# Kernel optimization log

Measured on AMD Instinct MI355X. Metric: run time of the kernel, lower is better.

The kernel has to match this reference:

```python
import jax, jax.numpy as jnp
import numpy as np

EPS = 1e-6  # torch GaussianNLLLoss default eps


def _linear_params(key, in_size, out_size):
    # torch nn.Linear default init: U(-1/sqrt(in), 1/sqrt(in)) for W and b
    kw, kb = jax.random.split(key)
    bound = 1.0 / np.sqrt(in_size)
    W = jax.random.uniform(kw, (out_size, in_size), minval=-bound, maxval=bound, dtype=jnp.float32)
    b = jax.random.uniform(kb, (out_size,), minval=-bound, maxval=bound, dtype=jnp.float32)
    return W, b


def setup_inputs() -> dict:
    key = jax.random.key(0)
    B, IN, H = 32768, 512, 512
    ks = jax.random.split(key, 6)
    x = jax.random.normal(ks[0], (B, IN), dtype=jnp.float32)
    y = jax.random.normal(ks[1], (B, IN), dtype=jnp.float32)
    W_mu_x, b_mu_x = _linear_params(ks[2], IN, H)
    W_sg_x, b_sg_x = _linear_params(ks[3], IN, H)
    W_mu_y, b_mu_y = _linear_params(ks[4], IN, H)
    W_sg_y, b_sg_y = _linear_params(ks[5], IN, H)
    return {"x": x, "y": y,
            "W_mu_x": W_mu_x, "b_mu_x": b_mu_x,
            "W_sg_x": W_sg_x, "b_sg_x": b_sg_x,
            "W_mu_y": W_mu_y, "b_mu_y": b_mu_y,
            "W_sg_y": W_sg_y, "b_sg_y": b_sg_y}


def _gaussian_nll(xi, mean, var):
    # torch GaussianNLLLoss (full=False, reduction='mean'):
    # mean over features of 0.5*(log(max(var,eps)) + (xi-mean)^2/max(var,eps))
    v = jnp.maximum(var, EPS)
    return 0.5 * jnp.mean(jnp.log(v) + (xi - mean) ** 2 / v)


def _sample_row(key, mx, my, vx, vy):
    # rejection sampling: draw u~U(0,1), xi~U(-1,1); accept when u >= q(xi)
    def cond(c):
        return jnp.logical_not(c[2])

    def body(c):
        k = c[0]
        k, k1, k2 = jax.random.split(k, 3)
        u = jax.random.uniform(k1, dtype=jnp.float32)
        xi = 2.0 * jax.random.uniform(k2, dtype=jnp.float32) - 1.0
        q = _gaussian_nll(xi, mx, vx) * _gaussian_nll(xi, my, vy)
        return (k, xi, u >= q)

    _, xi, _ = jax.lax.while_loop(cond, body, (key, jnp.float32(0.0), jnp.bool_(False)))
    return xi


def reference(x, y, W_mu_x, b_mu_x, W_sg_x, b_sg_x, W_mu_y, b_mu_y, W_sg_y, b_sg_y):
    mean_x = x @ W_mu_x.T + b_mu_x          # [B, H]
    mean_y = y @ W_mu_y.T + b_mu_y          # [B, H]
    std_x = jnp.exp(x @ W_sg_x.T + b_sg_x)  # [B, H] (used as 'var' in GaussianNLLLoss)
    std_y = jnp.exp(y @ W_sg_y.T + b_sg_y)  # [B, H]
    B = x.shape[0]
    keys = jax.random.split(jax.random.key(42), B)
    X = jax.vmap(_sample_row)(keys, mean_x, mean_y, std_x, std_y)  # [B]
    return jnp.clip(X, 1e-5, 10.0)
```

## Files before the change

kernel.cpp:

```cpp
#include <hip/hip_runtime.h>
#include <stdint.h>
#include <math.h>


typedef _Float16 f16;
typedef __attribute__((ext_vector_type(8))) _Float16 f16x8;
typedef __attribute__((ext_vector_type(4))) float f32x4;

#define SX 16.0f
#define SW 1024.0f
#define INV_S (1.0f / 16384.0f)
#define LOG_EPS (-13.815510557964274f)
#define PLANE 262144
#define WS_NEED (4u * 2u * PLANE * 2u)

#define KC_S   512
#define CJ_S   8192
#define WV_S   16384
#define CG_S   65536
#define HILO_S 262144
#define MAT_S  524288

struct U2 { uint32_t a, b; };

__device__ __forceinline__ uint32_t rotl(uint32_t v, int d) {
  return (v << d) | (v >> (32 - d));
}

__device__ __forceinline__ U2 tf2x32(uint32_t k0, uint32_t k1, uint32_t x0, uint32_t x1) {
  const uint32_t k2 = k0 ^ k1 ^ 0x1BD11BDAu;
  x0 += k0; x1 += k1;
#define TFR(r) { x0 += x1; x1 = rotl(x1, r); x1 ^= x0; }
  TFR(13) TFR(15) TFR(26) TFR(6)
  x0 += k1; x1 += k2 + 1u;
  TFR(17) TFR(29) TFR(16) TFR(24)
  x0 += k2; x1 += k0 + 2u;
  TFR(13) TFR(15) TFR(26) TFR(6)
  x0 += k0; x1 += k1 + 3u;
  TFR(17) TFR(29) TFR(16) TFR(24)
  x0 += k1; x1 += k2 + 4u;
  TFR(13) TFR(15) TFR(26) TFR(6)
  x0 += k2; x1 += k0 + 5u;
#undef TFR
  U2 r; r.a = x0; r.b = x1; return r;
}

__device__ __forceinline__ float bits_to_u01(uint32_t b) {
  return __uint_as_float((b >> 9) | 0x3f800000u) - 1.0f;
}

__global__ __launch_bounds__(256) void convert_w_kernel(
    const float* __restrict__ w0, const float* __restrict__ w1,
    const float* __restrict__ w2, const float* __restrict__ w3,
    f16* __restrict__ ws)
{
  const int t = blockIdx.x * 256 + threadIdx.x;
  const int mat = t >> 15;
  const int r = t & 32767;
  const int lane = r & 63;
  const int kc = (r >> 6) & 15;
  const int cj = (r >> 10) & 1;
  const int wv = (r >> 11) & 3;
  const int cg = (r >> 13) & 3;
  const int ln = lane & 15, quad = lane >> 4;
  const int row = cg * 128 + wv * 32 + cj * 16 + ln;
  const int k0 = kc * 32 + quad * 8;
  const float* W = (mat == 0) ? w0 : (mat == 1) ? w1 : (mat == 2) ? w2 : w3;
  const float* p = W + (size_t)row * 512 + k0;
  const float4 va = *(const float4*)p;
  const float4 vb = *(const float4*)(p + 4);
  const float a[8] = {va.x, va.y, va.z, va.w, vb.x, vb.y, vb.z, vb.w};
  f16x8 h, l;
#pragma unroll
  for (int i = 0; i < 8; ++i) {
    const float ai = a[i] * SW;
    const f16 hi = (f16)ai;
    h[i] = hi;
    l[i] = (f16)(ai - (float)hi);
  }
  f16* dst = ws + (size_t)mat * MAT_S + (size_t)cg * CG_S + (size_t)wv * WV_S
                + (size_t)cj * CJ_S + (size_t)kc * KC_S + (size_t)lane * 8;
  *(f16x8*)dst = h;
  *(f16x8*)(dst + HILO_S) = l;
}

__device__ __forceinline__ int swz_off(int row, int quad) {
  return row * 32 + ((quad ^ ((row >> 1) & 3)) << 3);
}

__global__ __launch_bounds__(256, 2)
void mfma_proposal_kernel(const float* __restrict__ gx, const float* __restrict__ gy,
                          const float* __restrict__ bmux, const float* __restrict__ bsgx,
                          const float* __restrict__ bmuy, const float* __restrict__ bsgy,
                          const f16* __restrict__ ws, float* __restrict__ out)
{
  __shared__ f16 Xh[64 * 32], Xl[64 * 32];
  __shared__ double red[4][64][8];

  const int tid = threadIdx.x;
  const int lane = tid & 63;
  const int w = tid >> 6;
  const int ln = lane & 15;
  const int quad = lane >> 4;
  const int r0 = blockIdx.x * 64;

  const int xrow = tid >> 2;
  const int xs4 = tid & 3;
  const int xslot = (xs4 ^ ((xrow >> 1) & 3)) << 3;

  for (int i = tid; i < 4 * 64 * 8; i += 256) (&red[0][0][0])[i] = 0.0;

  const f16* wbase = ws + (size_t)w * WV_S + (size_t)lane * 8;

  float4 xr0, xr1;
  auto load_xr = [&](int n) {
    const float* Xg = (n >> 6) ? gy : gx;
    const float* xp = Xg + (size_t)(r0 + xrow) * 512 + (n & 15) * 32 + xs4 * 8;
    xr0 = *(const float4*)(xp);
    xr1 = *(const float4*)(xp + 4);
  };

  auto write_x = [&]() {
    float a0 = xr0.x * SX, a1 = xr0.y * SX, a2 = xr0.z * SX, a3 = xr0.w * SX;
    float a4 = xr1.x * SX, a5 = xr1.y * SX, a6 = xr1.z * SX, a7 = xr1.w * SX;
    f16 h0 = (f16)a0, h1 = (f16)a1, h2 = (f16)a2, h3 = (f16)a3;
    f16 h4 = (f16)a4, h5 = (f16)a5, h6 = (f16)a6, h7 = (f16)a7;
    *(f16x8*)&Xh[xrow * 32 + xslot] = (f16x8){h0, h1, h2, h3, h4, h5, h6, h7};
    *(f16x8*)&Xl[xrow * 32 + xslot] =
        (f16x8){(f16)(a0 - (float)h0), (f16)(a1 - (float)h1),
                (f16)(a2 - (float)h2), (f16)(a3 - (float)h3),
                (f16)(a4 - (float)h4), (f16)(a5 - (float)h5),
                (f16)(a6 - (float)h6), (f16)(a7 - (float)h7)};
  };

  auto load_W = [&](int n, f16x8 (&B)[4][2]) {
    const int kc = n & 15, cg = (n >> 4) & 3, d = n >> 6;
    const f16* base = wbase + (size_t)(d * 2) * MAT_S + (size_t)cg * CG_S
                            + (size_t)kc * KC_S;
#pragma unroll
    for (int p = 0; p < 4; ++p)
#pragma unroll
      for (int cj = 0; cj < 2; ++cj)
        B[p][cj] = *(const f16x8*)(base + (size_t)(p >> 1) * MAT_S
                                        + (size_t)(p & 1) * HILO_S
                                        + (size_t)cj * CJ_S);
  };

  f16x8 Ba[4][2], Bb[4][2];
  f32x4 accm[4][2], accv[4][2];

  load_xr(0);
  load_W(0, Ba);

  auto round_fn = [&](int rid, f16x8 (&Bc)[4][2], f16x8 (&Bn)[4][2]) {
    const int kc = rid & 15;
    const int cg = (rid >> 4) & 3;
    const int dist = rid >> 6;

    if (kc == 0) {
#pragma unroll
      for (int ri = 0; ri < 4; ++ri)
#pragma unroll
        for (int cj = 0; cj < 2; ++cj) {
          accm[ri][cj] = (f32x4)0.0f;
          accv[ri][cj] = (f32x4)0.0f;
        }
    }

    __syncthreads();
    write_x();
    __syncthreads();

    if (rid + 1 < 128) {
      load_xr(rid + 1);
      load_W(rid + 1, Bn);
    }

    f16x8 ah[4], al[4];
#pragma unroll
    for (int ri = 0; ri < 4; ++ri) {
      const int off = swz_off(ri * 16 + ln, quad);
      ah[ri] = *(const f16x8*)&Xh[off];
      al[ri] = *(const f16x8*)&Xl[off];
    }
#pragma unroll
    for (int cj = 0; cj < 2; ++cj) {
      const f16x8 bhm = Bc[0][cj];
      const f16x8 blm = Bc[1][cj];
      const f16x8 bhv = Bc[2][cj];
      const f16x8 blv = Bc[3][cj];
#pragma unroll
      for (int ri = 0; ri < 4; ++ri) {
        accm[ri][cj] = __builtin_amdgcn_mfma_f32_16x16x32_f16(al[ri], bhm, accm[ri][cj], 0, 0, 0);
        accm[ri][cj] = __builtin_amdgcn_mfma_f32_16x16x32_f16(ah[ri], blm, accm[ri][cj], 0, 0, 0);
        accm[ri][cj] = __builtin_amdgcn_mfma_f32_16x16x32_f16(ah[ri], bhm, accm[ri][cj], 0, 0, 0);
        accv[ri][cj] = __builtin_amdgcn_mfma_f32_16x16x32_f16(al[ri], bhv, accv[ri][cj], 0, 0, 0);
        accv[ri][cj] = __builtin_amdgcn_mfma_f32_16x16x32_f16(ah[ri], blv, accv[ri][cj], 0, 0, 0);
        accv[ri][cj] = __builtin_amdgcn_mfma_f32_16x16x32_f16(ah[ri], bhv, accv[ri][cj], 0, 0, 0);
      }
    }

    if (kc == 15) {
      const float* bmu = dist ? bmuy : bmux;
      const float* bsg = dist ? bsgy : bsgx;
      float bm0 = bmu[cg * 128 + w * 32 + ln];
      float bm1 = bmu[cg * 128 + w * 32 + 16 + ln];
      float bv0 = bsg[cg * 128 + w * 32 + ln];
      float bv1 = bsg[cg * 128 + w * 32 + 16 + ln];
#pragma unroll
      for (int ri = 0; ri < 4; ++ri) {
#pragma unroll
        for (int g = 0; g < 4; ++g) {
          float pA = 0.f, pI = 0.f, pM = 0.f, pQ = 0.f;
#pragma unroll
          for (int cj = 0; cj < 2; ++cj) {
            const float m = accm[ri][cj][g] * INV_S + (cj ? bm1 : bm0);
            const float s = accv[ri][cj][g] * INV_S + (cj ? bv1 : bv0);
            const float vv = fmaxf(expf(s), 1e-6f);
            const float lg = fmaxf(s, LOG_EPS);
            const float iv = __builtin_amdgcn_rcpf(vv);
            pA += lg;
            pI += iv;
            pM += m * iv;
            pQ += m * m * iv;
          }
#pragma unroll
          for (int msk = 1; msk < 16; msk <<= 1) {
            pA += __shfl_xor(pA, msk);
            pI += __shfl_xor(pI, msk);
            pM += __shfl_xor(pM, msk);
            pQ += __shfl_xor(pQ, msk);
          }
          if (ln == 0) {
            double* rr = &red[w][ri * 16 + quad * 4 + g][dist * 4];
            rr[0] += (double)pA; rr[1] += (double)pI;
            rr[2] += (double)pM; rr[3] += (double)pQ;
          }
        }
      }
    }
  };

  for (int rr = 0; rr < 64; ++rr) {
    round_fn(rr * 2,     Ba, Bb);
    round_fn(rr * 2 + 1, Bb, Ba);
  }

  __syncthreads();

  if (tid < 64) {
    const int grow = r0 + tid;
    double Ax = 0, Ix = 0, Mx = 0, Qx = 0, Ay = 0, Iy = 0, My = 0, Qy = 0;
#pragma unroll
    for (int s = 0; s < 4; ++s) {
      Ax += red[s][tid][0]; Ix += red[s][tid][1];
      Mx += red[s][tid][2]; Qx += red[s][tid][3];
      Ay += red[s][tid][4]; Iy += red[s][tid][5];
      My += red[s][tid][6]; Qy += red[s][tid][7];
    }

    U2 key = tf2x32(0u, 42u, 0u, (uint32_t)grow);

    float xi = 0.0f;
    bool done = false;
    for (int it = 0; it < 100000 && !done; ++it) {
      const U2 kn = tf2x32(key.a, key.b, 0u, 0u);
      const U2 k1 = tf2x32(key.a, key.b, 0u, 1u);
      const U2 k2 = tf2x32(key.a, key.b, 0u, 2u);
      const U2 ru = tf2x32(k1.a, k1.b, 0u, 0u);
      const U2 rx = tf2x32(k2.a, k2.b, 0u, 0u);
      const float u  = bits_to_u01(ru.a ^ ru.b);
      const float u2 = bits_to_u01(rx.a ^ rx.b);
      xi = 2.0f * u2 - 1.0f;
      const double dxi = (double)xi;
      const double nx = (0.5 / 512.0) * (Ax + Qx + dxi * (dxi * Ix - 2.0 * Mx));
      const double ny = (0.5 / 512.0) * (Ay + Qy + dxi * (dxi * Iy - 2.0 * My));
      done = ((double)u >= nx * ny);
      key = kn;
    }
    out[grow] = fminf(fmaxf(xi, 1e-5f), 10.0f);
  }
}

__global__ __launch_bounds__(256, 1)
void fused_proposal_vec(const float* __restrict__ gx, const float* __restrict__ gy,
                        const float* __restrict__ Wmux, const float* __restrict__ bmux,
                        const float* __restrict__ Wsgx, const float* __restrict__ bsgx,
                        const float* __restrict__ Wmuy, const float* __restrict__ bmuy,
                        const float* __restrict__ Wsgy, const float* __restrict__ bsgy,
                        float* __restrict__ out)
{
  __shared__ float Xs[16][68];
  __shared__ float Wms[16][132];
  __shared__ float Wss[16][132];
  __shared__ double red[64][8];

  const int tid = threadIdx.x;
  const int tx = tid & 15;
  const int ty = tid >> 4;
  const int r0 = blockIdx.x * 64;
  const int lr = tid >> 2;
  const int q4 = (tid & 3) << 2;

  for (int i = tid; i < 64 * 8; i += 256) ((double*)red)[i] = 0.0;

  for (int ph = 0; ph < 8; ++ph) {
    const int dist = ph >> 2;
    const int c0 = (ph & 3) * 128;
    const float* __restrict__ Xg = dist ? gy : gx;
    const float* __restrict__ Wm = dist ? Wmuy : Wmux;
    const float* __restrict__ Wv = dist ? Wsgy : Wsgx;
    const float* __restrict__ bm = dist ? bmuy : bmux;
    const float* __restrict__ bv = dist ? bsgy : bsgx;

    float am[4][8], av[4][8];
#pragma unroll
    for (int r = 0; r < 4; ++r)
#pragma unroll
      for (int c = 0; c < 8; ++c) { am[r][c] = 0.0f; av[r][c] = 0.0f; }

    const float* xp  = Xg + (size_t)(r0 + lr) * 512 + q4;
    const float* mp0 = Wm + (size_t)(c0 + lr) * 512 + q4;
    const float* mp1 = Wm + (size_t)(c0 + lr + 64) * 512 + q4;
    const float* vp0 = Wv + (size_t)(c0 + lr) * 512 + q4;
    const float* vp1 = Wv + (size_t)(c0 + lr + 64) * 512 + q4;

    float4 xa = *(const float4*)(xp);
    float4 ma = *(const float4*)(mp0);
    float4 mb = *(const float4*)(mp1);
    float4 va = *(const float4*)(vp0);
    float4 vb = *(const float4*)(vp1);

    for (int t = 0; t < 32; ++t) {
      __syncthreads();
#define ST4(arr, col, v) { arr[q4+0][col]=v.x; arr[q4+1][col]=v.y; arr[q4+2][col]=v.z; arr[q4+3][col]=v.w; }
      ST4(Xs,  lr, xa)
      ST4(Wms, lr, ma)  ST4(Wms, lr + 64, mb)
      ST4(Wss, lr, va)  ST4(Wss, lr + 64, vb)
#undef ST4
      __syncthreads();
      if (t + 1 < 32) {
        const int ko = (t + 1) * 16;
        xa = *(const float4*)(xp + ko);
        ma = *(const float4*)(mp0 + ko);
        mb = *(const float4*)(mp1 + ko);
        va = *(const float4*)(vp0 + ko);
        vb = *(const float4*)(vp1 + ko);
      }
#pragma unroll
      for (int kk = 0; kk < 16; ++kk) {
        const float4 x0 = *(const float4*)&Xs[kk][ty * 4];
        const float4 m0 = *(const float4*)&Wms[kk][tx * 4];
        const float4 m1 = *(const float4*)&Wms[kk][tx * 4 + 64];
        const float4 v0 = *(const float4*)&Wss[kk][tx * 4];
        const float4 v1 = *(const float4*)&Wss[kk][tx * 4 + 64];
        const float xr[4] = {x0.x, x0.y, x0.z, x0.w};
        const float wm[8] = {m0.x, m0.y, m0.z, m0.w, m1.x, m1.y, m1.z, m1.w};
        const float wv[8] = {v0.x, v0.y, v0.z, v0.w, v1.x, v1.y, v1.z, v1.w};
#pragma unroll
        for (int r = 0; r < 4; ++r)
#pragma unroll
          for (int c = 0; c < 8; ++c) {
            am[r][c] = fmaf(xr[r], wm[c], am[r][c]);
            av[r][c] = fmaf(xr[r], wv[c], av[r][c]);
          }
      }
    }

    float bmr[8], bvr[8];
#pragma unroll
    for (int c = 0; c < 4; ++c) {
      bmr[c]     = bm[c0 + tx * 4 + c];
      bmr[4 + c] = bm[c0 + 64 + tx * 4 + c];
      bvr[c]     = bv[c0 + tx * 4 + c];
      bvr[4 + c] = bv[c0 + 64 + tx * 4 + c];
    }
#pragma unroll
    for (int r = 0; r < 4; ++r) {
      float pA = 0.f, pI = 0.f, pM = 0.f, pQ = 0.f;
#pragma unroll
      for (int c = 0; c < 8; ++c) {
        const float m = am[r][c] + bmr[c];
        const float s = av[r][c] + bvr[c];
        const float v = fmaxf(expf(s), 1e-6f);
        const float lg = fmaxf(s, LOG_EPS);
        const float inv = __builtin_amdgcn_rcpf(v);
        pA += lg; pI += inv; pM += m * inv; pQ += m * m * inv;
      }
#pragma unroll
      for (int msk = 1; msk < 16; msk <<= 1) {
        pA += __shfl_xor(pA, msk);
        pI += __shfl_xor(pI, msk);
        pM += __shfl_xor(pM, msk);
        pQ += __shfl_xor(pQ, msk);
      }
      if (tx == 0) {
        double* rr = &red[ty * 4 + r][dist * 4];
        rr[0] += (double)pA; rr[1] += (double)pI;
        rr[2] += (double)pM; rr[3] += (double)pQ;
      }
    }
  }

  __syncthreads();

  if (tid < 64) {
    const int grow = r0 + tid;
    const double Ax = red[tid][0], Ix = red[tid][1], Mx = red[tid][2], Qx = red[tid][3];
    const double Ay = red[tid][4], Iy = red[tid][5], My = red[tid][6], Qy = red[tid][7];
    U2 key = tf2x32(0u, 42u, 0u, (uint32_t)grow);
    float xi = 0.0f;
    bool done = false;
    for (int it = 0; it < 100000 && !done; ++it) {
      const U2 kn = tf2x32(key.a, key.b, 0u, 0u);
      const U2 k1 = tf2x32(key.a, key.b, 0u, 1u);
      const U2 k2 = tf2x32(key.a, key.b, 0u, 2u);
      const U2 ru = tf2x32(k1.a, k1.b, 0u, 0u);
      const U2 rx = tf2x32(k2.a, k2.b, 0u, 0u);
      const float u  = bits_to_u01(ru.a ^ ru.b);
      const float u2 = bits_to_u01(rx.a ^ rx.b);
      xi = 2.0f * u2 - 1.0f;
      const double dxi = (double)xi;
      const double nx = (0.5 / 512.0) * (Ax + Qx + dxi * (dxi * Ix - 2.0 * Mx));
      const double ny = (0.5 / 512.0) * (Ay + Qy + dxi * (dxi * Iy - 2.0 * My));
      done = ((double)u >= nx * ny);
      key = kn;
    }
    out[grow] = fminf(fmaxf(xi, 1e-5f), 10.0f);
  }
}

extern "C" void kernel_launch(void* const* d_in, const int* in_sizes, int n_in,
                              void* d_out, int out_size, void* d_ws, size_t ws_size,
                              hipStream_t stream) {
  const float* x    = (const float*)d_in[0];
  const float* y    = (const float*)d_in[1];
  const float* Wmux = (const float*)d_in[2];
  const float* bmux = (const float*)d_in[3];
  const float* Wsgx = (const float*)d_in[4];
  const float* bsgx = (const float*)d_in[5];
  const float* Wmuy = (const float*)d_in[6];
  const float* bmuy = (const float*)d_in[7];
  const float* Wsgy = (const float*)d_in[8];
  const float* bsgy = (const float*)d_in[9];
  (void)in_sizes; (void)n_in; (void)out_size;

  if (ws_size >= (size_t)WS_NEED) {
    convert_w_kernel<<<512, 256, 0, stream>>>(Wmux, Wsgx, Wmuy, Wsgy, (f16*)d_ws);
    mfma_proposal_kernel<<<512, 256, 0, stream>>>(
        x, y, bmux, bsgx, bmuy, bsgy, (const f16*)d_ws, (float*)d_out);
  } else {
    fused_proposal_vec<<<512, 256, 0, stream>>>(
        x, y, Wmux, bmux, Wsgx, bsgx, Wmuy, bmuy, Wsgy, bsgy, (float*)d_out);
  }
}
```

Baseline: 367.8 us.

## Halve rows per block, double-buffer X tile, raise occupancy to four blocks

Each block now handles 32 rows instead of 64, with twice as many blocks and launch bounds raised to four blocks per CU. The X tile in LDS is double-buffered so only one barrier is needed per round, and register double-buffering of W fragments is replaced by per-round loads. The intent is more waves to hide latency and fewer barriers, at the cost of halved W reuse per block and therefore more L2/global weight traffic.

```diff
diff --git a/kernel.cpp b/kernel.cpp
--- a/kernel.cpp
+++ b/kernel.cpp
@@ -88,78 +88,70 @@
   return row * 32 + ((quad ^ ((row >> 1) & 3)) << 3);
 }
 
-__global__ __launch_bounds__(256, 2)
+__global__ __launch_bounds__(256, 4)
 void mfma_proposal_kernel(const float* __restrict__ gx, const float* __restrict__ gy,
                           const float* __restrict__ bmux, const float* __restrict__ bsgx,
                           const float* __restrict__ bmuy, const float* __restrict__ bsgy,
                           const f16* __restrict__ ws, float* __restrict__ out)
 {
-  __shared__ f16 Xh[64 * 32], Xl[64 * 32];
-  __shared__ double red[4][64][8];
+  __shared__ f16 Xh[2][32 * 32], Xl[2][32 * 32];
+  __shared__ double red[4][32][8];
 
   const int tid = threadIdx.x;
   const int lane = tid & 63;
   const int w = tid >> 6;
   const int ln = lane & 15;
   const int quad = lane >> 4;
-  const int r0 = blockIdx.x * 64;
-
-  const int xrow = tid >> 2;
+  const int r0 = blockIdx.x * 32;
+
+  const int xrow = (tid & 127) >> 2;
   const int xs4 = tid & 3;
   const int xslot = (xs4 ^ ((xrow >> 1) & 3)) << 3;
 
-  for (int i = tid; i < 4 * 64 * 8; i += 256) (&red[0][0][0])[i] = 0.0;
+  for (int i = tid; i < 4 * 32 * 8; i += 256) (&red[0][0][0])[i] = 0.0;
 
   const f16* wbase = ws + (size_t)w * WV_S + (size_t)lane * 8;
 
   float4 xr0, xr1;
   auto load_xr = [&](int n) {
-    const float* Xg = (n >> 6) ? gy : gx;
-    const float* xp = Xg + (size_t)(r0 + xrow) * 512 + (n & 15) * 32 + xs4 * 8;
-    xr0 = *(const float4*)(xp);
-    xr1 = *(const float4*)(xp + 4);
+    if (w < 2) {
+      const float* Xg = (n >> 6) ? gy : gx;
+      const float* xp = Xg + (size_t)(r0 + xrow) * 512 + (n & 15) * 32 + xs4 * 8;
+      xr0 = *(const float4*)(xp);
+      xr1 = *(const float4*)(xp + 4);
+    }
   };
 
-  auto write_x = [&]() {
-    float a0 = xr0.x * SX, a1 = xr0.y * SX, a2 = xr0.z * SX, a3 = xr0.w * SX;
-    float a4 = xr1.x * SX, a5 = xr1.y * SX, a6 = xr1.z * SX, a7 = xr1.w * SX;
-    f16 h0 = (f16)a0, h1 = (f16)a1, h2 = (f16)a2, h3 = (f16)a3;
-    f16 h4 = (f16)a4, h5 = (f16)a5, h6 = (f16)a6, h7 = (f16)a7;
-    *(f16x8*)&Xh[xrow * 32 + xslot] = (f16x8){h0, h1, h2, h3, h4, h5, h6, h7};
-    *(f16x8*)&Xl[xrow * 32 + xslot] =
-        (f16x8){(f16)(a0 - (float)h0), (f16)(a1 - (float)h1),
-                (f16)(a2 - (float)h2), (f16)(a3 - (float)h3),
-                (f16)(a4 - (float)h4), (f16)(a5 - (float)h5),
-                (f16)(a6 - (float)h6), (f16)(a7 - (float)h7)};
+  auto write_x = [&](int buf) {
+    if (w < 2) {
+      float a0 = xr0.x * SX, a1 = xr0.y * SX, a2 = xr0.z * SX, a3 = xr0.w * SX;
+      float a4 = xr1.x * SX, a5 = xr1.y * SX, a6 = xr1.z * SX, a7 = xr1.w * SX;
+      f16 h0 = (f16)a0, h1 = (f16)a1, h2 = (f16)a2, h3 = (f16)a3;
+      f16 h4 = (f16)a4, h5 = (f16)a5, h6 = (f16)a6, h7 = (f16)a7;
+      *(f16x8*)&Xh[buf][xrow * 32 + xslot] = (f16x8){h0, h1, h2, h3, h4, h5, h6, h7};
+      *(f16x8*)&Xl[buf][xrow * 32 + xslot] =
+          (f16x8){(f16)(a0 - (float)h0), (f16)(a1 - (float)h1),
+                  (f16)(a2 - (float)h2), (f16)(a3 - (float)h3),
+                  (f16)(a4 - (float)h4), (f16)(a5 - (float)h5),
+                  (f16)(a6 - (float)h6), (f16)(a7 - (float)h7)};
+    }
   };
 
-  auto load_W = [&](int n, f16x8 (&B)[4][2]) {
-    const int kc = n & 15, cg = (n >> 4) & 3, d = n >> 6;
-    const f16* base = wbase + (size_t)(d * 2) * MAT_S + (size_t)cg * CG_S
-                            + (size_t)kc * KC_S;
-#pragma unroll
-    for (int p = 0; p < 4; ++p)
-#pragma unroll
-      for (int cj = 0; cj < 2; ++cj)
-        B[p][cj] = *(const f16x8*)(base + (size_t)(p >> 1) * MAT_S
-                                        + (size_t)(p & 1) * HILO_S
-                                        + (size_t)cj * CJ_S);
-  };
-
-  f16x8 Ba[4][2], Bb[4][2];
-  f32x4 accm[4][2], accv[4][2];
+  f32x4 accm[2][2], accv[2][2];
 
   load_xr(0);
-  load_W(0, Ba);
-
-  auto round_fn = [&](int rid, f16x8 (&Bc)[4][2], f16x8 (&Bn)[4][2]) {
+  write_x(0);
+  load_xr(1);
+
+  for (int rid = 0; rid < 128; ++rid) {
+    const int cb = rid & 1;
     const int kc = rid & 15;
     const int cg = (rid >> 4) & 3;
     const int dist = rid >> 6;
 
     if (kc == 0) {
 #pragma unroll
-      for (int ri = 0; ri < 4; ++ri)
+      for (int ri = 0; ri < 2; ++ri)
 #pragma unroll
         for (int cj = 0; cj < 2; ++cj) {
           accm[ri][cj] = (f32x4)0.0f;
@@ -168,29 +160,38 @@
     }
 
     __syncthreads();
-    write_x();
-    __syncthreads();
-
-    if (rid + 1 < 128) {
-      load_xr(rid + 1);
-      load_W(rid + 1, Bn);
-    }
-
-    f16x8 ah[4], al[4];
-#pragma unroll
-    for (int ri = 0; ri < 4; ++ri) {
+
+    if (rid + 1 < 128) write_x(cb ^ 1);
+    if (rid + 2 < 128) load_xr(rid + 2);
+
+    f16x8 B[4][2];
+    {
+      const f16* base = wbase + (size_t)(dist * 2) * MAT_S + (size_t)cg * CG_S
+                              + (size_t)kc * KC_S;
+#pragma unroll
+      for (int p = 0; p < 4; ++p)
+#pragma unroll
+        for (int cj = 0; cj < 2; ++cj)
+          B[p][cj] = *(const f16x8*)(base + (size_t)(p >> 1) * MAT_S
+                                          + (size_t)(p & 1) * HILO_S
+                                          + (size_t)cj * CJ_S);
+    }
+
+    f16x8 ah[2], al[2];
+#pragma unroll
+    for (int ri = 0; ri < 2; ++ri) {
       const int off = swz_off(ri * 16 + ln, quad);
-      ah[ri] = *(const f16x8*)&Xh[off];
-      al[ri] = *(const f16x8*)&Xl[off];
+      ah[ri] = *(const f16x8*)&Xh[cb][off];
+      al[ri] = *(const f16x8*)&Xl[cb][off];
     }
 #pragma unroll
     for (int cj = 0; cj < 2; ++cj) {
-      const f16x8 bhm = Bc[0][cj];
-      const f16x8 blm = Bc[1][cj];
-      const f16x8 bhv = Bc[2][cj];
-      const f16x8 blv = Bc[3][cj];
-#pragma unroll
-      for (int ri = 0; ri < 4; ++ri) {
+      const f16x8 bhm = B[0][cj];
+      const f16x8 blm = B[1][cj];
+      const f16x8 bhv = B[2][cj];
+      const f16x8 blv = B[3][cj];
+#pragma unroll
+      for (int ri = 0; ri < 2; ++ri) {
         accm[ri][cj] = __builtin_amdgcn_mfma_f32_16x16x32_f16(al[ri], bhm, accm[ri][cj], 0, 0, 0);
         accm[ri][cj] = __builtin_amdgcn_mfma_f32_16x16x32_f16(ah[ri], blm, accm[ri][cj], 0, 0, 0);
         accm[ri][cj] = __builtin_amdgcn_mfma_f32_16x16x32_f16(ah[ri], bhm, accm[ri][cj], 0, 0, 0);
@@ -208,7 +209,7 @@
       float bv0 = bsg[cg * 128 + w * 32 + ln];
       float bv1 = bsg[cg * 128 + w * 32 + 16 + ln];
 #pragma unroll
-      for (int ri = 0; ri < 4; ++ri) {
+      for (int ri = 0; ri < 2; ++ri) {
 #pragma unroll
         for (int g = 0; g < 4; ++g) {
           float pA = 0.f, pI = 0.f, pM = 0.f, pQ = 0.f;
@@ -239,16 +240,11 @@
         }
       }
     }
-  };
-
-  for (int rr = 0; rr < 64; ++rr) {
-    round_fn(rr * 2,     Ba, Bb);
-    round_fn(rr * 2 + 1, Bb, Ba);
   }
 
   __syncthreads();
 
-  if (tid < 64) {
+  if (tid < 32) {
     const int grow = r0 + tid;
     double Ax = 0, Ix = 0, Mx = 0, Qx = 0, Ay = 0, Iy = 0, My = 0, Qy = 0;
 #pragma unroll
@@ -447,7 +443,7 @@
 
   if (ws_size >= (size_t)WS_NEED) {
     convert_w_kernel<<<512, 256, 0, stream>>>(Wmux, Wsgx, Wmuy, Wsgy, (f16*)d_ws);
-    mfma_proposal_kernel<<<512, 256, 0, stream>>>(
+    mfma_proposal_kernel<<<1024, 256, 0, stream>>>(
         x, y, bmux, bsgx, bmuy, bsgy, (const f16*)d_ws, (float*)d_out);
   } else {
     fused_proposal_vec<<<512, 256, 0, stream>>>(
```

After: 386.7 us. 5.1% more time.

## Double-buffer X tiles in LDS and process K=64 per round

Applied to the files above, without the earlier changes.

The main loop now handles 64 K-elements per round instead of 32, halving the number of rounds and barriers. It double-buffers the converted X tiles in LDS so only one __syncthreads is needed per round. The weight workspace is re-laid out so each round's B fragments are contiguous, and they are loaded at the top of the round instead of being prefetched a round ahead. MFMA blocks are wrapped in s_setprio to favour matrix issue. The trade-offs are more LDS use, higher register pressure, and exposed weight-load latency because the register prefetch of B was removed.

```diff
diff --git a/kernel.cpp b/kernel.cpp
--- a/kernel.cpp
+++ b/kernel.cpp
@@ -11,15 +11,13 @@
 #define SW 1024.0f
 #define INV_S (1.0f / 16384.0f)
 #define LOG_EPS (-13.815510557964274f)
-#define PLANE 262144
-#define WS_NEED (4u * 2u * PLANE * 2u)
-
-#define KC_S   512
-#define CJ_S   8192
-#define WV_S   16384
-#define CG_S   65536
-#define HILO_S 262144
-#define MAT_S  524288
+#define WS_NEED (4u * 1024u * 1024u)
+
+#define L_CJ    512
+#define L_WV    1024
+#define L_PL    4096
+#define L_KS    16384
+#define L_RID   32768
 
 struct U2 { uint32_t a, b; };
 
@@ -55,16 +53,20 @@
     f16* __restrict__ ws)
 {
   const int t = blockIdx.x * 256 + threadIdx.x;
-  const int mat = t >> 15;
-  const int r = t & 32767;
-  const int lane = r & 63;
-  const int kc = (r >> 6) & 15;
-  const int cj = (r >> 10) & 1;
-  const int wv = (r >> 11) & 3;
-  const int cg = (r >> 13) & 3;
-  const int ln = lane & 15, quad = lane >> 4;
-  const int row = cg * 128 + wv * 32 + cj * 16 + ln;
-  const int k0 = kc * 32 + quad * 8;
+  const int lane = t & 63;
+  const int cj = (t >> 6) & 1;
+  const int wv = (t >> 7) & 3;
+  const int matsel = (t >> 9) & 1;
+  const int ksub = (t >> 10) & 1;
+  const int rid = t >> 11;
+  const int dist = rid >> 5;
+  const int cg = (rid >> 3) & 3;
+  const int kc2 = rid & 7;
+
+  const int mat = dist * 2 + matsel;
+  const int row = cg * 128 + wv * 32 + cj * 16 + (lane & 15);
+  const int k0 = kc2 * 64 + ksub * 32 + (lane >> 4) * 8;
+
   const float* W = (mat == 0) ? w0 : (mat == 1) ? w1 : (mat == 2) ? w2 : w3;
   const float* p = W + (size_t)row * 512 + k0;
   const float4 va = *(const float4*)p;
@@ -78,10 +80,11 @@
     h[i] = hi;
     l[i] = (f16)(ai - (float)hi);
   }
-  f16* dst = ws + (size_t)mat * MAT_S + (size_t)cg * CG_S + (size_t)wv * WV_S
-                + (size_t)cj * CJ_S + (size_t)kc * KC_S + (size_t)lane * 8;
+  f16* dst = ws + (size_t)rid * L_RID + (size_t)ksub * L_KS
+                + (size_t)(matsel * 2) * L_PL + (size_t)wv * L_WV
+                + (size_t)cj * L_CJ + (size_t)lane * 8;
   *(f16x8*)dst = h;
-  *(f16x8*)(dst + HILO_S) = l;
+  *(f16x8*)(dst + L_PL) = l;
 }
 
 __device__ __forceinline__ int swz_off(int row, int quad) {
@@ -94,7 +97,8 @@
                           const float* __restrict__ bmuy, const float* __restrict__ bsgy,
                           const f16* __restrict__ ws, float* __restrict__ out)
 {
-  __shared__ f16 Xh[64 * 32], Xl[64 * 32];
+  __shared__ f16 Xh[2][2][64 * 32];
+  __shared__ f16 Xl[2][2][64 * 32];
   __shared__ double red[4][64][8];
 
   const int tid = threadIdx.x;
@@ -110,54 +114,48 @@
 
   for (int i = tid; i < 4 * 64 * 8; i += 256) (&red[0][0][0])[i] = 0.0;
 
-  const f16* wbase = ws + (size_t)w * WV_S + (size_t)lane * 8;
-
-  float4 xr0, xr1;
+  float4 xr0a, xr0b, xr1a, xr1b;
+
   auto load_xr = [&](int n) {
-    const float* Xg = (n >> 6) ? gy : gx;
-    const float* xp = Xg + (size_t)(r0 + xrow) * 512 + (n & 15) * 32 + xs4 * 8;
-    xr0 = *(const float4*)(xp);
-    xr1 = *(const float4*)(xp + 4);
+    const float* Xg = (n >> 5) ? gy : gx;
+    const float* xp = Xg + (size_t)(r0 + xrow) * 512 + (n & 7) * 64 + xs4 * 8;
+    xr0a = *(const float4*)(xp);
+    xr0b = *(const float4*)(xp + 4);
+    xr1a = *(const float4*)(xp + 32);
+    xr1b = *(const float4*)(xp + 36);
   };
 
-  auto write_x = [&]() {
-    float a0 = xr0.x * SX, a1 = xr0.y * SX, a2 = xr0.z * SX, a3 = xr0.w * SX;
-    float a4 = xr1.x * SX, a5 = xr1.y * SX, a6 = xr1.z * SX, a7 = xr1.w * SX;
-    f16 h0 = (f16)a0, h1 = (f16)a1, h2 = (f16)a2, h3 = (f16)a3;
-    f16 h4 = (f16)a4, h5 = (f16)a5, h6 = (f16)a6, h7 = (f16)a7;
-    *(f16x8*)&Xh[xrow * 32 + xslot] = (f16x8){h0, h1, h2, h3, h4, h5, h6, h7};
-    *(f16x8*)&Xl[xrow * 32 + xslot] =
-        (f16x8){(f16)(a0 - (float)h0), (f16)(a1 - (float)h1),
-                (f16)(a2 - (float)h2), (f16)(a3 - (float)h3),
-                (f16)(a4 - (float)h4), (f16)(a5 - (float)h5),
-                (f16)(a6 - (float)h6), (f16)(a7 - (float)h7)};
+  auto write_x = [&](int buf) {
+#pragma unroll
+    for (int s = 0; s < 2; ++s) {
+      const float4 ra = s ? xr1a : xr0a;
+      const float4 rb = s ? xr1b : xr0b;
+      float a0 = ra.x * SX, a1 = ra.y * SX, a2 = ra.z * SX, a3 = ra.w * SX;
+      float a4 = rb.x * SX, a5 = rb.y * SX, a6 = rb.z * SX, a7 = rb.w * SX;
+      f16 h0 = (f16)a0, h1 = (f16)a1, h2 = (f16)a2, h3 = (f16)a3;
+      f16 h4 = (f16)a4, h5 = (f16)a5, h6 = (f16)a6, h7 = (f16)a7;
+      *(f16x8*)&Xh[buf][s][xrow * 32 + xslot] = (f16x8){h0, h1, h2, h3, h4, h5, h6, h7};
+      *(f16x8*)&Xl[buf][s][xrow * 32 + xslot] =
+          (f16x8){(f16)(a0 - (float)h0), (f16)(a1 - (float)h1),
+                  (f16)(a2 - (float)h2), (f16)(a3 - (float)h3),
+                  (f16)(a4 - (float)h4), (f16)(a5 - (float)h5),
+                  (f16)(a6 - (float)h6), (f16)(a7 - (float)h7)};
+    }
   };
 
-  auto load_W = [&](int n, f16x8 (&B)[4][2]) {
-    const int kc = n & 15, cg = (n >> 4) & 3, d = n >> 6;
-    const f16* base = wbase + (size_t)(d * 2) * MAT_S + (size_t)cg * CG_S
-                            + (size_t)kc * KC_S;
-#pragma unroll
-    for (int p = 0; p < 4; ++p)
-#pragma unroll
-      for (int cj = 0; cj < 2; ++cj)
-        B[p][cj] = *(const f16x8*)(base + (size_t)(p >> 1) * MAT_S
-                                        + (size_t)(p & 1) * HILO_S
-                                        + (size_t)cj * CJ_S);
-  };
-
-  f16x8 Ba[4][2], Bb[4][2];
   f32x4 accm[4][2], accv[4][2];
 
   load_xr(0);
-  load_W(0, Ba);
-
-  auto round_fn = [&](int rid, f16x8 (&Bc)[4][2], f16x8 (&Bn)[4][2]) {
-    const int kc = rid & 15;
-    const int cg = (rid >> 4) & 3;
-    const int dist = rid >> 6;
-
-    if (kc == 0) {
+  write_x(0);
+  load_xr(1);
+
+  for (int rid = 0; rid < 64; ++rid) {
+    const int cb = rid & 1;
+    const int kc2 = rid & 7;
+    const int cg = (rid >> 3) & 3;
+    const int dist = rid >> 5;
+
+    if (kc2 == 0) {
 #pragma unroll
       for (int ri = 0; ri < 4; ++ri)
 #pragma unroll
@@ -168,39 +166,50 @@
     }
 
     __syncthreads();
-    write_x();
-    __syncthreads();
-
-    if (rid + 1 < 128) {
-      load_xr(rid + 1);
-      load_W(rid + 1, Bn);
-    }
-
-    f16x8 ah[4], al[4];
-#pragma unroll
-    for (int ri = 0; ri < 4; ++ri) {
-      const int off = swz_off(ri * 16 + ln, quad);
-      ah[ri] = *(const f16x8*)&Xh[off];
-      al[ri] = *(const f16x8*)&Xl[off];
-    }
-#pragma unroll
-    for (int cj = 0; cj < 2; ++cj) {
-      const f16x8 bhm = Bc[0][cj];
-      const f16x8 blm = Bc[1][cj];
-      const f16x8 bhv = Bc[2][cj];
-      const f16x8 blv = Bc[3][cj];
+
+    const f16* wr = ws + (size_t)rid * L_RID + (size_t)w * L_WV + (size_t)lane * 8;
+    f16x8 B0[4][2], B1[4][2];
+#pragma unroll
+    for (int p = 0; p < 4; ++p)
+#pragma unroll
+      for (int cj = 0; cj < 2; ++cj) {
+        B0[p][cj] = *(const f16x8*)(wr + (size_t)p * L_PL + (size_t)cj * L_CJ);
+        B1[p][cj] = *(const f16x8*)(wr + L_KS + (size_t)p * L_PL + (size_t)cj * L_CJ);
+      }
+
+    if (rid + 1 < 64) write_x(cb ^ 1);
+    if (rid + 2 < 64) load_xr(rid + 2);
+
+#pragma unroll
+    for (int s = 0; s < 2; ++s) {
+      f16x8 ah[4], al[4];
 #pragma unroll
       for (int ri = 0; ri < 4; ++ri) {
-        accm[ri][cj] = __builtin_amdgcn_mfma_f32_16x16x32_f16(al[ri], bhm, accm[ri][cj], 0, 0, 0);
-        accm[ri][cj] = __builtin_amdgcn_mfma_f32_16x16x32_f16(ah[ri], blm, accm[ri][cj], 0, 0, 0);
-        accm[ri][cj] = __builtin_amdgcn_mfma_f32_16x16x32_f16(ah[ri], bhm, accm[ri][cj], 0, 0, 0);
-        accv[ri][cj] = __builtin_amdgcn_mfma_f32_16x16x32_f16(al[ri], bhv, accv[ri][cj], 0, 0, 0);
-        accv[ri][cj] = __builtin_amdgcn_mfma_f32_16x16x32_f16(ah[ri], blv, accv[ri][cj], 0, 0, 0);
-        accv[ri][cj] = __builtin_amdgcn_mfma_f32_16x16x32_f16(ah[ri], bhv, accv[ri][cj], 0, 0, 0);
-      }
-    }
-
-    if (kc == 15) {
+        const int off = swz_off(ri * 16 + ln, quad);
+        ah[ri] = *(const f16x8*)&Xh[cb][s][off];
+        al[ri] = *(const f16x8*)&Xl[cb][s][off];
+      }
+      __builtin_amdgcn_s_setprio(1);
+#pragma unroll
+      for (int cj = 0; cj < 2; ++cj) {
+        const f16x8 bhm = s ? B1[0][cj] : B0[0][cj];
+        const f16x8 blm = s ? B1[1][cj] : B0[1][cj];
+        const f16x8 bhv = s ? B1[2][cj] : B0[2][cj];
+        const f16x8 blv = s ? B1[3][cj] : B0[3][cj];
+#pragma unroll
+        for (int ri = 0; ri < 4; ++ri) {
+          accm[ri][cj] = __builtin_amdgcn_mfma_f32_16x16x32_f16(al[ri], bhm, accm[ri][cj], 0, 0, 0);
+          accm[ri][cj] = __builtin_amdgcn_mfma_f32_16x16x32_f16(ah[ri], blm, accm[ri][cj], 0, 0, 0);
+          accm[ri][cj] = __builtin_amdgcn_mfma_f32_16x16x32_f16(ah[ri], bhm, accm[ri][cj], 0, 0, 0);
+          accv[ri][cj] = __builtin_amdgcn_mfma_f32_16x16x32_f16(al[ri], bhv, accv[ri][cj], 0, 0, 0);
+          accv[ri][cj] = __builtin_amdgcn_mfma_f32_16x16x32_f16(ah[ri], blv, accv[ri][cj], 0, 0, 0);
+          accv[ri][cj] = __builtin_amdgcn_mfma_f32_16x16x32_f16(ah[ri], bhv, accv[ri][cj], 0, 0, 0);
+        }
+      }
+      __builtin_amdgcn_s_setprio(0);
+    }
+
+    if (kc2 == 7) {
       const float* bmu = dist ? bmuy : bmux;
       const float* bsg = dist ? bsgy : bsgx;
       float bm0 = bmu[cg * 128 + w * 32 + ln];
@@ -239,11 +248,6 @@
         }
       }
     }
-  };
-
-  for (int rr = 0; rr < 64; ++rr) {
-    round_fn(rr * 2,     Ba, Bb);
-    round_fn(rr * 2 + 1, Bb, Ba);
   }
 
   __syncthreads();
```

Measured after the change: 355.6 us. 3.3% less time.
